# Kernel tuning notes

Hardware: AMD Instinct MI355X
Metric: run time of the kernel (lower is better)

The kernel has to match this reference:

```python
import jax, jax.numpy as jnp
import numpy as np

P, L, H = 4, 32, 1024          # path_num, layers_num, lstm_size
TEMP, TANH_C = 5.0, 2.5        # temperature, controller_tanh_constant


def setup_inputs() -> dict:
    key = jax.random.key(0)
    ks = jax.random.split(key, 8)
    s = 0.05  # mimics nn.init.uniform_(-0.1, 0.1) scale
    return {
        "emb": jax.random.normal(ks[0], (P, L + 1, H), jnp.float32) * s,
        "w_ih": jax.random.normal(ks[1], (P, 4 * H, H), jnp.float32) * s,
        "w_hh": jax.random.normal(ks[2], (P, 4 * H, H), jnp.float32) * s,
        "b_ih": jax.random.normal(ks[3], (P, 4 * H), jnp.float32) * s,
        "b_hh": jax.random.normal(ks[4], (P, 4 * H), jnp.float32) * s,
        "w_attn1": jax.random.normal(ks[5], (P, H, H), jnp.float32) * s,
        "w_attn2": jax.random.normal(ks[6], (P, H, H), jnp.float32) * s,
        "w_index": jax.random.normal(ks[7], (P, H), jnp.float32) * s,
        "seed": 0,
    }


def _lstm_cell(w_ih_p, w_hh_p, b_ih_p, b_hh_p, x, h, c):
    # torch.nn.LSTMCell: gates ordered i, f, g, o
    g = w_ih_p @ x + b_ih_p + w_hh_p @ h + b_hh_p  # [4H]
    i, f, gg, o = jnp.split(g, 4)
    i, f, o = jax.nn.sigmoid(i), jax.nn.sigmoid(f), jax.nn.sigmoid(o)
    c2 = f * c + i * jnp.tanh(gg)
    return o * jnp.tanh(c2), c2


def _forward(emb, w_ih, w_hh, b_ih, b_hh, w_attn1, w_attn2, w_index, seed):
    base_key = jax.random.key(seed)
    h = [jnp.zeros((H,), emb.dtype) for _ in range(P)]
    c = [jnp.zeros((H,), emb.dtype) for _ in range(P)]
    anchors = []  # list of [H] anchor_w_1 vectors, grows by P each layer
    # warm-up step: feed the <layers_num> token through each path's LSTM
    for p in range(P):
        h[p], c[p] = _lstm_cell(w_ih[p], w_hh[p], b_ih[p], b_hh[p], emb[p, L], h[p], c[p])
        anchors.append(w_attn1[p] @ h[p])
    arch, ents, lps = [], [], []
    node_index = None  # carried across ALL inner steps, as in the torch loop var
    for l in range(L):
        pre_query = jnp.stack(anchors)  # [P*(l+1), H]
        cur = []
        for p in range(P):
            if l == 0:
                x = emb[p, L]
            else:
                x = emb[node_index % P, node_index // P]  # data-dependent gather
            h[p], c[p] = _lstm_cell(w_ih[p], w_hh[p], b_ih[p], b_hh[p], x, h[p], c[p])
            anchor = w_attn2[p] @ h[p]
            cur.append(w_attn1[p] @ h[p])
            q = jnp.tanh(pre_query + anchor)          # [n, H]
            logits = (q @ w_index[p]) / TEMP          # [n]
            logits = TANH_C * jnp.tanh(logits)
            step_key = jax.random.fold_in(base_key, l * P + p)
            idx = jax.random.categorical(step_key, logits)  # == multinomial(softmax)
            logp = jax.nn.log_softmax(logits)
            lps.append(-logp[idx])  # F.cross_entropy with a single target
            ents.append(jax.lax.stop_gradient(-jnp.sum(jnp.exp(logp) * logp)))
            arch.append(idx)
            node_index = idx
        anchors += cur
    arch_seq = jnp.stack(arch)
    entropy = sum(ents)
    log_prob = sum(lps)
    return arch_seq % P, arch_seq // P, entropy, log_prob


def reference(emb, w_ih, w_hh, b_ih, b_hh, w_attn1, w_attn2, w_index, seed):
    return _forward(emb, w_ih, w_hh, b_ih, b_hh, w_attn1, w_attn2, w_index, seed)
```

## Files before the change

### kernel.cpp

```cpp
#include <hip/hip_runtime.h>
#include <stdint.h>
#include <math.h>

#define P_     4
#define L_     32
#define H_     1024
#define NE_    132
#define G4_    4096
#define TEMP_  5.0f
#define TANHC_ 2.5f
#define TINY_  1.1754943508222875e-38f

#define PRNG_PARTITIONABLE 1

#define NBLK   256
#define NTHR   512
#define NFUSE  64
#define WBASE  65

__device__ __forceinline__ uint64_t pk(float v, uint32_t s) {
  union { float f; uint32_t u; } c; c.f = v;
  return ((uint64_t)s << 32) | c.u;
}
__device__ __forceinline__ float upk(uint64_t w) {
  union { uint32_t u; float f; } c; c.u = (uint32_t)w; return c.f;
}
__device__ __forceinline__ uint64_t ald64(const uint64_t* p) {
  return __hip_atomic_load(p, __ATOMIC_RELAXED, __HIP_MEMORY_SCOPE_AGENT);
}
__device__ __forceinline__ void ast64(uint64_t* p, uint64_t v) {
  __hip_atomic_store(p, v, __ATOMIC_RELAXED, __HIP_MEMORY_SCOPE_AGENT);
}
__device__ __forceinline__ void at_stf(float* p, float v) {
  __hip_atomic_store(p, v, __ATOMIC_RELAXED, __HIP_MEMORY_SCOPE_AGENT);
}
__device__ __forceinline__ int at_ldi(const int* p) {
  return __hip_atomic_load(p, __ATOMIC_RELAXED, __HIP_MEMORY_SCOPE_AGENT);
}
__device__ __forceinline__ void vmwait() {
  asm volatile("s_waitcnt vmcnt(0)" ::: "memory");
}

__device__ __forceinline__ float wave_reduce_sum(float v) {
  for (int off = 32; off; off >>= 1) v += __shfl_xor(v, off);
  return v;
}
__device__ __forceinline__ float sigmoidf_(float x) {
  return 0.5f + 0.5f * tanhf(0.5f * x);
}
__device__ __forceinline__ void tf2x32(uint32_t k0, uint32_t k1,
                                       uint32_t& x0, uint32_t& x1) {
  uint32_t ks2 = k0 ^ k1 ^ 0x1BD11BDAu;
  x0 += k0; x1 += k1;
#define RR(r) { x0 += x1; x1 = (x1 << r) | (x1 >> (32 - r)); x1 ^= x0; }
  RR(13) RR(15) RR(26) RR(6)
  x0 += k1;  x1 += ks2 + 1u;
  RR(17) RR(29) RR(16) RR(24)
  x0 += ks2; x1 += k0 + 2u;
  RR(13) RR(15) RR(26) RR(6)
  x0 += k0;  x1 += k1 + 3u;
  RR(17) RR(29) RR(16) RR(24)
  x0 += k1;  x1 += ks2 + 4u;
  RR(13) RR(15) RR(26) RR(6)
  x0 += ks2; x1 += k0 + 5u;
#undef RR
}
__device__ __forceinline__ float dot_core(const float* __restrict__ wrow,
                                          const float* hv, int lane) {
  float acc = 0.f;
  for (int it = 0; it < 4; ++it) {
    float4 w4 = *(const float4*)(wrow + lane * 4 + it * 256);
    float4 h4 = *(const float4*)(hv   + lane * 4 + it * 256);
    acc += w4.x * h4.x + w4.y * h4.y + w4.z * h4.z + w4.w * h4.w;
  }
  return wave_reduce_sum(acc);
}

__global__ __launch_bounds__(256) void k_pre(const float* __restrict__ emb,
                                             const float* __restrict__ w_ih,
                                             const float* __restrict__ b_ih,
                                             const float* __restrict__ b_hh,
                                             float* __restrict__ Xp,
                                             int* __restrict__ adone) {
  int blk  = blockIdx.x;
  if (blk == 0 && threadIdx.x < 128) adone[threadIdx.x] = 0;
  int p    = blk >> 8;
  int rg   = blk & 255;
  int wave = threadIdx.x >> 6;
  int lane = threadIdx.x & 63;
  int r0   = rg * 16 + wave * 4;

  const float* wbase = w_ih + ((size_t)p * G4_ + r0) * H_;
  float4 Wr[4][4];
  for (int q = 0; q < 4; ++q)
    for (int it = 0; it < 4; ++it)
      Wr[q][it] = *(const float4*)(wbase + (size_t)q * H_ + lane * 4 + it * 256);
  float bias[4];
  for (int q = 0; q < 4; ++q)
    bias[q] = b_ih[p * G4_ + r0 + q] + b_hh[p * G4_ + r0 + q];

  for (int e = 0; e < NE_; ++e) {
    const float* ev = emb + (size_t)e * H_;
    float4 x[4];
    for (int it = 0; it < 4; ++it)
      x[it] = *(const float4*)(ev + lane * 4 + it * 256);
    for (int q = 0; q < 4; ++q) {
      float acc = 0.f;
      for (int it = 0; it < 4; ++it)
        acc += Wr[q][it].x * x[it].x + Wr[q][it].y * x[it].y
             + Wr[q][it].z * x[it].z + Wr[q][it].w * x[it].w;
      acc = wave_reduce_sum(acc);
      if (lane == 0)
        Xp[((size_t)p * NE_ + e) * G4_ + r0 + q] = acc + bias[q];
    }
  }
}

struct KA {
  const float *Xp, *w_hh, *w_a1, *w_a2, *w_idx;
  const int* seed;
  uint64_t *hst;
  uint64_t *Gst;
  float    *anc;
  int      *adone;
  uint64_t *a2st;
  uint64_t *lst;
  float *out;
};

__global__ __launch_bounds__(NTHR) void k_main(KA a) {
  const int blk  = blockIdx.x;
  const int tid  = threadIdx.x;
  const int wave = tid >> 6;
  const int lane = tid & 63;
  __shared__ __align__(16) float lds[4096];
  __shared__ int sh_i;

  if (blk == 0) {
    for (int p = 0; p < P_; ++p) {
      const float* g = a.Xp + ((size_t)p * NE_ + (p * 33 + 32)) * G4_;
      for (int k = 0; k < 2; ++k) {
        int j = tid + k * 512;
        float c2 = sigmoidf_(g[j]) * tanhf(g[j + 2048]);
        float h2 = sigmoidf_(g[j + 3072]) * tanhf(c2);
        lds[p * H_ + j] = c2;
        ast64(a.hst + (size_t)p * H_ + j, pk(h2, p + 1));
      }
    }
    if (tid == 0) sh_i = 0;
    __syncthreads();

    float ent_acc = 0.f, lp_acc = 0.f;
    for (int s = 0; s < 128; ++s) {
      const int l = s >> 2, p = s & 3, n = 4 * (l + 1);
      const uint32_t st = (uint32_t)(s + 1);
      int idx = sh_i;
      int e = (l == 0) ? (p * 33 + 32) : ((idx & 3) * 33 + (idx >> 2));
      const float* xrow = a.Xp + ((size_t)p * NE_ + e) * G4_;
      const uint64_t* Gp = a.Gst + (size_t)p * G4_;

      uint64_t wv[8]; float xv[8]; float cold[2];
      for (int k = 0; k < 2; ++k) {
        int j = tid + k * 512;
        for (int q = 0; q < 4; ++q) {
          wv[k * 4 + q] = ald64(Gp + j + q * 1024);
          xv[k * 4 + q] = xrow[j + q * 1024];
        }
        cold[k] = lds[p * H_ + j];
      }
      for (int k = 0; k < 2; ++k)
        for (int q = 0; q < 4; ++q) {
          int j = tid + k * 512;
          while ((uint32_t)(wv[k * 4 + q] >> 32) != st)
            wv[k * 4 + q] = ald64(Gp + j + q * 1024);
        }
      __syncthreads();
      for (int k = 0; k < 2; ++k) {
        int j = tid + k * 512;
        float gi = upk(wv[k * 4 + 0]) + xv[k * 4 + 0];
        float gf = upk(wv[k * 4 + 1]) + xv[k * 4 + 1];
        float gg = upk(wv[k * 4 + 2]) + xv[k * 4 + 2];
        float go = upk(wv[k * 4 + 3]) + xv[k * 4 + 3];
        float c2 = sigmoidf_(gf) * cold[k] + sigmoidf_(gi) * tanhf(gg);
        float h2 = sigmoidf_(go) * tanhf(c2);
        lds[p * H_ + j] = c2;
        ast64(a.hst + (size_t)p * H_ + j, pk(h2, (uint32_t)(s + 5)));
      }

      if (wave == 0) {
        uint64_t lw[2]; int ii[2]; float lg[2], sv[2];
        for (int k = 0; k < 2; ++k) {
          int i = lane + 64 * k; ii[k] = i;
          if (i < n) lw[k] = ald64(a.lst + i);
        }
        for (int k = 0; k < 2; ++k)
          if (ii[k] < n)
            while ((uint32_t)(lw[k] >> 32) != st) lw[k] = ald64(a.lst + ii[k]);
        uint32_t seed = (uint32_t)(*a.seed);
        uint32_t sk0 = 0u, sk1 = (uint32_t)s;
        tf2x32(0u, seed, sk0, sk1);
        for (int k = 0; k < 2; ++k) {
          int i = ii[k];
          if (i < n) {
#if PRNG_PARTITIONABLE
            uint32_t b0 = 0u, b1 = (uint32_t)i;
            tf2x32(sk0, sk1, b0, b1);
            uint32_t bits = b0 ^ b1;
#else
            int half = n >> 1;
            uint32_t c0 = (uint32_t)(i < half ? i : i - half);
            uint32_t c1 = (uint32_t)(i < half ? i + half : i);
            uint32_t r0 = c0, r1 = c1;
            tf2x32(sk0, sk1, r0, r1);
            uint32_t bits = (i < half) ? r0 : r1;
#endif
            uint32_t fb = (bits >> 9) | 0x3F800000u;
            float u = __uint_as_float(fb) - 1.0f;
            u = fmaxf(TINY_, u * (1.0f - TINY_) + TINY_);
            float g = -logf(-logf(u));
            lg[k] = upk(lw[k]);
            sv[k] = g + lg[k];
          } else { sv[k] = -INFINITY; lg[k] = -INFINITY; }
        }
        float bv; int bi;
        if (sv[0] >= sv[1]) { bv = sv[0]; bi = ii[0]; }
        else                { bv = sv[1]; bi = ii[1]; }
        for (int off = 32; off; off >>= 1) {
          float ov = __shfl_xor(bv, off);
          int   oi = __shfl_xor(bi, off);
          if (ov > bv || (ov == bv && oi < bi)) { bv = ov; bi = oi; }
        }
        float m = fmaxf(lg[0], lg[1]);
        for (int off = 32; off; off >>= 1) m = fmaxf(m, __shfl_xor(m, off));
        float se = 0.f;
        for (int k = 0; k < 2; ++k) if (ii[k] < n) se += expf(lg[k] - m);
        se = wave_reduce_sum(se);
        float lse = logf(se);
        float ent = 0.f;
        for (int k = 0; k < 2; ++k) if (ii[k] < n) {
          float lpv = (lg[k] - m) - lse;
          ent -= expf(lpv) * lpv;
        }
        ent = wave_reduce_sum(ent);
        if (lane == 0) {
          float li = (bi == ii[0]) ? lg[0] : __shfl(lg[1], bi - 64);
          li = upk(ald64(a.lst + bi));
          ent_acc += ent;
          lp_acc  += -((li - m) - lse);
          a.out[s]       = (float)(bi & 3);
          a.out[128 + s] = (float)(bi >> 2);
          sh_i = bi;
        }
      }
      __syncthreads();
    }
    if (tid == 0) { a.out[256] = ent_acc; a.out[257] = lp_acc; }

  } else if (blk <= NFUSE) {
    const int fb = blk - 1;
    float4 areg[4]; bool haveA = false;
    const int rl = 2 * fb + wave;
    for (int s = 0; s < 128; ++s) {
      const int p = s & 3, n = 4 * ((s >> 2) + 1);
      const uint32_t st = (uint32_t)(s + 1);
      const uint32_t hs = (uint32_t)(s + 5);
      __syncthreads();
      {
        const uint64_t* hp = a.hst + (size_t)p * H_;
        uint64_t w0 = ald64(hp + tid), w1 = ald64(hp + tid + 512);
        while ((uint32_t)(w0 >> 32) != hs) w0 = ald64(hp + tid);
        while ((uint32_t)(w1 >> 32) != hs) w1 = ald64(hp + tid + 512);
        lds[tid] = upk(w0); lds[tid + 512] = upk(w1);
      }
      __syncthreads();
      for (int q = 0; q < 2; ++q) {
        int r = fb * 16 + wave * 2 + q;
        float v = dot_core(a.w_a2 + ((size_t)p * H_ + r) * H_, lds, lane);
        if (lane == 0) ast64(a.a2st + r, pk(v, st));
      }
      bool active = (2 * fb) < n;
      if (active) {
        if (wave < 2 && !haveA && rl < n) {
          while (at_ldi(a.adone + rl) < H_) __builtin_amdgcn_s_sleep(1);
          const float* ar = a.anc + (size_t)rl * H_;
          for (int it = 0; it < 4; ++it)
            areg[it] = *(const float4*)(ar + lane * 4 + it * 256);
          haveA = true;
        }
        {
          uint64_t w0 = ald64(a.a2st + tid), w1 = ald64(a.a2st + tid + 512);
          while ((uint32_t)(w0 >> 32) != st) w0 = ald64(a.a2st + tid);
          while ((uint32_t)(w1 >> 32) != st) w1 = ald64(a.a2st + tid + 512);
          lds[1024 + tid] = upk(w0); lds[1024 + tid + 512] = upk(w1);
        }
        __syncthreads();
        if (wave < 2 && rl < n) {
          const float* wi = a.w_idx + p * H_;
          float acc = 0.f;
          for (int it = 0; it < 4; ++it) {
            float4 a4 = areg[it];
            float4 b4 = *(const float4*)(&lds[1024 + lane * 4 + it * 256]);
            float4 w4 = *(const float4*)(wi + lane * 4 + it * 256);
            acc += tanhf(a4.x + b4.x) * w4.x + tanhf(a4.y + b4.y) * w4.y
                 + tanhf(a4.z + b4.z) * w4.z + tanhf(a4.w + b4.w) * w4.w;
          }
          acc = wave_reduce_sum(acc);
          if (lane == 0) ast64(a.lst + rl, pk(TANHC_ * tanhf(acc / TEMP_), st));
        }
      }
    }

  } else {
    const int x  = blk - WBASE;
    const int p  = x & 3;
    const int w  = x >> 2;
    const int nw = (p < 3) ? 48 : 47;
    const int aLo = w * H_  / nw, aHi = (w + 1) * H_  / nw;
    const int gLo = w * G4_ / nw, gHi = (w + 1) * G4_ / nw;
    const float* wa = a.w_a1 + (size_t)p * H_  * H_;
    const float* wg = a.w_hh + (size_t)p * G4_ * H_;
    for (int ev = p; ev < 128; ev += 4) {
      const uint32_t st = (uint32_t)(ev + 1);
      const uint64_t* hp = a.hst + (size_t)(ev & 3) * H_;
      __syncthreads();
      {
        uint64_t w0 = ald64(hp + tid), w1 = ald64(hp + tid + 512);
        while ((uint32_t)(w0 >> 32) != st) {
          __builtin_amdgcn_s_sleep(1); w0 = ald64(hp + tid);
        }
        while ((uint32_t)(w1 >> 32) != st) {
          __builtin_amdgcn_s_sleep(1); w1 = ald64(hp + tid + 512);
        }
        lds[tid] = upk(w0); lds[tid + 512] = upk(w1);
      }
      __syncthreads();
      float* ad = a.anc + (size_t)ev * H_;
      for (int d = aLo + wave; d < aHi; d += 8) {
        float v = dot_core(wa + (size_t)d * H_, lds, lane);
        if (lane == 0) at_stf(ad + d, v);
      }
      vmwait();
      __syncthreads();
      if (tid == 0) atomicAdd(a.adone + ev, aHi - aLo);
      uint64_t* gd = a.Gst + (size_t)(ev & 3) * G4_;
      for (int d = gLo + wave; d < gHi; d += 8) {
        float v = dot_core(wg + (size_t)d * H_, lds, lane);
        if (lane == 0) ast64(gd + d, pk(v, st));
      }
    }
  }
}

extern "C" void kernel_launch(void* const* d_in, const int* in_sizes, int n_in,
                              void* d_out, int out_size, void* d_ws, size_t ws_size,
                              hipStream_t stream) {
  (void)in_sizes; (void)n_in; (void)out_size; (void)ws_size;
  const float* emb   = (const float*)d_in[0];
  const float* w_ih  = (const float*)d_in[1];
  const float* w_hh  = (const float*)d_in[2];
  const float* b_ih  = (const float*)d_in[3];
  const float* b_hh  = (const float*)d_in[4];
  const float* w_a1  = (const float*)d_in[5];
  const float* w_a2  = (const float*)d_in[6];
  const float* w_idx = (const float*)d_in[7];
  const int*   seed  = (const int*)d_in[8];
  float* out = (float*)d_out;

  float* ws = (float*)d_ws;
  size_t o = 0;
  float*    Xp   = ws + o;              o += (size_t)P_ * NE_ * G4_;
  uint64_t* hst  = (uint64_t*)(ws + o); o += 2 * 4 * H_;
  uint64_t* Gst  = (uint64_t*)(ws + o); o += 2 * 4 * G4_;
  float*    anc  = ws + o;              o += (size_t)128 * H_;
  uint64_t* a2st = (uint64_t*)(ws + o); o += 2 * H_;
  uint64_t* lst  = (uint64_t*)(ws + o); o += 2 * 128;
  int*      adn  = (int*)(ws + o);      o += 128;

  k_pre<<<1024, 256, 0, stream>>>(emb, w_ih, b_ih, b_hh, Xp, adn);

  KA ka;
  ka.Xp = Xp; ka.w_hh = w_hh; ka.w_a1 = w_a1; ka.w_a2 = w_a2; ka.w_idx = w_idx;
  ka.seed = seed;
  ka.hst = hst; ka.Gst = Gst; ka.anc = anc; ka.adone = adn;
  ka.a2st = a2st; ka.lst = lst; ka.out = out;

  void* kp[] = { (void*)&ka };
  hipLaunchCooperativeKernel((const void*)k_main, dim3(NBLK), dim3(NTHR),
                             kp, 0, stream);
}
```

Measured before the change: 1.765 ms.

## Batch four matvec rows per wave and rebalance fuse/worker block split

Adds a dot_core4 helper that loads four weight rows at once and reuses the same hidden-vector loads, so each wave has more memory loads in flight in the attention and recurrent matvecs. Halves the number of fused attention/logit blocks (each now covers four rows per wave) and gives the freed blocks to the w_a1/w_hh worker pool. The intent is to cut latency per sequential step through more memory-level parallelism and a better block balance. It costs more registers, and the heavier per-block work in the fused blocks could lengthen the critical path.

```diff
diff --git a/kernel.cpp b/kernel.cpp
--- a/kernel.cpp
+++ b/kernel.cpp
@@ -15,8 +15,8 @@
 
 #define NBLK   256
 #define NTHR   512
-#define NFUSE  64
-#define WBASE  65
+#define NFUSE  32
+#define WBASE  33
 
 __device__ __forceinline__ uint64_t pk(float v, uint32_t s) {
   union { float f; uint32_t u; } c; c.f = v;
@@ -74,6 +74,27 @@
     acc += w4.x * h4.x + w4.y * h4.y + w4.z * h4.z + w4.w * h4.w;
   }
   return wave_reduce_sum(acc);
+}
+__device__ __forceinline__ void dot_core4(const float* __restrict__ wbase,
+                                          size_t rstride,
+                                          const float* hv, int lane,
+                                          float o[4]) {
+  float4 w[4][4]; float4 h4[4];
+  for (int it = 0; it < 4; ++it) {
+    int off = lane * 4 + it * 256;
+    w[0][it] = *(const float4*)(wbase + off);
+    w[1][it] = *(const float4*)(wbase + rstride + off);
+    w[2][it] = *(const float4*)(wbase + 2 * rstride + off);
+    w[3][it] = *(const float4*)(wbase + 3 * rstride + off);
+    h4[it]   = *(const float4*)(hv + off);
+  }
+  for (int r = 0; r < 4; ++r) {
+    float acc = 0.f;
+    for (int it = 0; it < 4; ++it)
+      acc += w[r][it].x * h4[it].x + w[r][it].y * h4[it].y
+           + w[r][it].z * h4[it].z + w[r][it].w * h4[it].w;
+    o[r] = wave_reduce_sum(acc);
+  }
 }
 
 __global__ __launch_bounds__(256) void k_pre(const float* __restrict__ emb,
@@ -243,8 +264,7 @@
         }
         ent = wave_reduce_sum(ent);
         if (lane == 0) {
-          float li = (bi == ii[0]) ? lg[0] : __shfl(lg[1], bi - 64);
-          li = upk(ald64(a.lst + bi));
+          float li = upk(ald64(a.lst + bi));
           ent_acc += ent;
           lp_acc  += -((li - m) - lse);
           a.out[s]       = (float)(bi & 3);
@@ -259,7 +279,7 @@
   } else if (blk <= NFUSE) {
     const int fb = blk - 1;
     float4 areg[4]; bool haveA = false;
-    const int rl = 2 * fb + wave;
+    const int rl = 4 * fb + wave;
     for (int s = 0; s < 128; ++s) {
       const int p = s & 3, n = 4 * ((s >> 2) + 1);
       const uint32_t st = (uint32_t)(s + 1);
@@ -273,14 +293,16 @@
         lds[tid] = upk(w0); lds[tid + 512] = upk(w1);
       }
       __syncthreads();
-      for (int q = 0; q < 2; ++q) {
-        int r = fb * 16 + wave * 2 + q;
-        float v = dot_core(a.w_a2 + ((size_t)p * H_ + r) * H_, lds, lane);
-        if (lane == 0) ast64(a.a2st + r, pk(v, st));
-      }
-      bool active = (2 * fb) < n;
+      {
+        int r = fb * 32 + wave * 4;
+        float o[4];
+        dot_core4(a.w_a2 + ((size_t)p * H_ + r) * H_, H_, lds, lane, o);
+        if (lane == 0)
+          for (int q = 0; q < 4; ++q) ast64(a.a2st + r + q, pk(o[q], st));
+      }
+      bool active = (4 * fb) < n;
       if (active) {
-        if (wave < 2 && !haveA && rl < n) {
+        if (wave < 4 && !haveA && rl < n) {
           while (at_ldi(a.adone + rl) < H_) __builtin_amdgcn_s_sleep(1);
           const float* ar = a.anc + (size_t)rl * H_;
           for (int it = 0; it < 4; ++it)
@@ -294,7 +316,7 @@
           lds[1024 + tid] = upk(w0); lds[1024 + tid + 512] = upk(w1);
         }
         __syncthreads();
-        if (wave < 2 && rl < n) {
+        if (wave < 4 && rl < n) {
           const float* wi = a.w_idx + p * H_;
           float acc = 0.f;
           for (int it = 0; it < 4; ++it) {
@@ -314,7 +336,7 @@
     const int x  = blk - WBASE;
     const int p  = x & 3;
     const int w  = x >> 2;
-    const int nw = (p < 3) ? 48 : 47;
+    const int nw = (p < 3) ? 56 : 55;
     const int aLo = w * H_  / nw, aHi = (w + 1) * H_  / nw;
     const int gLo = w * G4_ / nw, gHi = (w + 1) * G4_ / nw;
     const float* wa = a.w_a1 + (size_t)p * H_  * H_;
@@ -335,17 +357,37 @@
       }
       __syncthreads();
       float* ad = a.anc + (size_t)ev * H_;
-      for (int d = aLo + wave; d < aHi; d += 8) {
-        float v = dot_core(wa + (size_t)d * H_, lds, lane);
-        if (lane == 0) at_stf(ad + d, v);
+      for (int d = aLo + wave * 4; d < aHi; d += 32) {
+        int m = aHi - d; m = m > 4 ? 4 : m;
+        if (m == 4) {
+          float o[4];
+          dot_core4(wa + (size_t)d * H_, H_, lds, lane, o);
+          if (lane == 0)
+            for (int q = 0; q < 4; ++q) at_stf(ad + d + q, o[q]);
+        } else {
+          for (int q = 0; q < m; ++q) {
+            float v = dot_core(wa + (size_t)(d + q) * H_, lds, lane);
+            if (lane == 0) at_stf(ad + d + q, v);
+          }
+        }
       }
       vmwait();
       __syncthreads();
       if (tid == 0) atomicAdd(a.adone + ev, aHi - aLo);
       uint64_t* gd = a.Gst + (size_t)(ev & 3) * G4_;
-      for (int d = gLo + wave; d < gHi; d += 8) {
-        float v = dot_core(wg + (size_t)d * H_, lds, lane);
-        if (lane == 0) ast64(gd + d, pk(v, st));
+      for (int d = gLo + wave * 4; d < gHi; d += 32) {
+        int m = gHi - d; m = m > 4 ? 4 : m;
+        if (m == 4) {
+          float o[4];
+          dot_core4(wg + (size_t)d * H_, H_, lds, lane, o);
+          if (lane == 0)
+            for (int q = 0; q < 4; ++q) ast64(gd + d + q, pk(o[q], st));
+        } else {
+          for (int q = 0; q < m; ++q) {
+            float v = dot_core(wg + (size_t)(d + q) * H_, lds, lane);
+            if (lane == 0) ast64(gd + d + q, pk(v, st));
+          }
+        }
       }
     }
   }
```

Measured after the change: 1.937 ms. 1.1x slower.
